# Optimization experiments

Hardware: AMD Instinct MI355X
Metric: run time of the kernel (lower is better)

The kernel has to match this reference:

```python
import jax, jax.numpy as jnp
import numpy as np

SCALE = 1.0 / np.sqrt(128.0)  # 1/sqrt(head_size)
NEG = -1000000000.0


def setup_inputs() -> dict:
    key = jax.random.key(0)
    k1, k2, k3, k4 = jax.random.split(key, 4)
    B, H, S, D = 2, 16, 2048, 128
    q = jax.random.normal(k1, (B, H, S, D), dtype=jnp.float32)
    k = jax.random.normal(k2, (B, H, S, D), dtype=jnp.float32)
    v = jax.random.normal(k3, (B, H, S, D), dtype=jnp.float32)
    mask = jax.random.randint(k4, (B, S), 0, 2, dtype=jnp.int32)
    return {"q": q, "k": k, "v": v, "mask": mask}


def reference(q, k, v, mask):
    # scores: [B, H, Sq, Sk]
    scores = jnp.einsum("bhqd,bhkd->bhqk", q, k) * SCALE
    m = mask[:, None, None, :]  # [B,1,1,Sk], broadcast over heads and queries
    scores = jnp.where(m == 0, NEG, scores)
    weights = jax.nn.softmax(scores, axis=-1)
    out = jnp.einsum("bhqk,bhkd->bhqd", weights, v)
    return out
```

## Files before the change

kernel.cpp:

```cpp
#include <hip/hip_runtime.h>
#include <hip/hip_bf16.h>

typedef __attribute__((ext_vector_type(8))) short short8;
typedef __attribute__((ext_vector_type(4))) short short4v;
typedef __attribute__((ext_vector_type(4))) float floatx4;

#define NBH 32
#define SS 2048
#define DD 128
#define BQ 128
#define BK 32
#define KTILES (SS / BK)
#define KPAIRS (KTILES / 2)
#define SCALE 0.08838834764831845f
#define LOG2E 1.4426950408889634f
#define MAXB 12.0f
#define MASKED_BIAS -100000.0f

#define WC_LGKM0 0xC07F

typedef union { float4 v; float f[4]; } f4u;

__device__ __forceinline__ short f2bf(float f) {
  union { float f; unsigned u; } x; x.f = f;
  return (short)((x.u + 0x7FFFu + ((x.u >> 16) & 1u)) >> 16);
}

__device__ __forceinline__ void pack8(short8* dst, float a, float b, float c, float d,
                                      float e, float f, float g, float h) {
  union { __hip_bfloat162 h2[4]; short8 v; } u;
  u.h2[0] = __float22bfloat162_rn(make_float2(a, b));
  u.h2[1] = __float22bfloat162_rn(make_float2(c, d));
  u.h2[2] = __float22bfloat162_rn(make_float2(e, f));
  u.h2[3] = __float22bfloat162_rn(make_float2(g, h));
  *dst = u.v;
}

__global__ __launch_bounds__(256, 2) void fa_kernel(
    const float* __restrict__ q, const float* __restrict__ k,
    const float* __restrict__ v, const int* __restrict__ mask,
    float* __restrict__ out) {
  __shared__ __align__(16) short Ks[4][BK * DD];
  __shared__ __align__(16) short Vt[4][DD * BK];
  __shared__ float Bias[SS];

  const int tid = threadIdx.x;
  const int wave = tid >> 6;
  const int lane = tid & 63;
  const int l16 = lane & 15;
  const int quad = lane >> 4;

  const int lid = blockIdx.y * 16 + blockIdx.x;
  const int vid = (lid & 7) * 64 + (lid >> 3);
  const int bh = vid >> 4;
  const int q0 = (vid & 15) * BQ;
  const int b = bh >> 4;
  const int poff = ((bh >> 1) & 1) << 4;

  const size_t base = (size_t)bh * SS * DD;
  const float* qg = q + base;
  const float* kg = k + base;
  const float* vg = v + base;
  const int* mg = mask + b * SS;
  const float c1 = SCALE * LOG2E, c2 = MAXB * LOG2E;

  const int krow = wave * 8 + (lane >> 3);
  const int kswr = krow & 7;
  const int kc0 = (lane & 7) * 2;
  const float* kldp = kg + (size_t)krow * DD + (lane & 7) * 16;
  const int kw0 = krow * DD + ((kc0 ^ kswr) * 8);
  const int kw1 = krow * DD + (((kc0 + 1) ^ kswr) * 8);
  const int kg4 = wave * 2 + (lane >> 5);
  const int dg = lane & 31;
  const int vgrp = kg4 & 3;
  const int vhalf = (kg4 >> 2) * 4;
  const float* vldp = vg + (size_t)(kg4 * 4) * DD + dg * 4;

  f4u kst[2][4], vst[2][4];

  {
    const int ktA = 2 * poff, ktB = ktA + 1;
#pragma unroll
    for (int i = 0; i < 4; ++i) {
      kst[0][i].v = *(const float4*)(kldp + (size_t)ktA * (BK * DD) + i * 4);
      kst[1][i].v = *(const float4*)(kldp + (size_t)ktB * (BK * DD) + i * 4);
    }
#pragma unroll
    for (int r = 0; r < 4; ++r) {
      vst[0][r].v = *(const float4*)(vldp + (size_t)ktA * (BK * DD) + r * DD);
      vst[1][r].v = *(const float4*)(vldp + (size_t)ktB * (BK * DD) + r * DD);
    }
  }

  short8 qf[2][4];
#pragma unroll
  for (int t = 0; t < 2; ++t) {
    const float* qp = qg + (size_t)(q0 + wave * 32 + t * 16 + l16) * DD;
#pragma unroll
    for (int dc = 0; dc < 4; ++dc) {
      float4 a = *(const float4*)(qp + dc * 32 + quad * 8);
      float4 bb = *(const float4*)(qp + dc * 32 + quad * 8 + 4);
      short8 tt;
      tt[0] = f2bf(a.x); tt[1] = f2bf(a.y); tt[2] = f2bf(a.z); tt[3] = f2bf(a.w);
      tt[4] = f2bf(bb.x); tt[5] = f2bf(bb.y); tt[6] = f2bf(bb.z); tt[7] = f2bf(bb.w);
      qf[t][dc] = tt;
    }
  }

  {
    int i0 = tid * 8;
    int4 m0 = *(const int4*)(mg + i0);
    int4 m1 = *(const int4*)(mg + i0 + 4);
    float4 f0, f1;
    f0.x = m0.x ? -c2 : MASKED_BIAS; f0.y = m0.y ? -c2 : MASKED_BIAS;
    f0.z = m0.z ? -c2 : MASKED_BIAS; f0.w = m0.w ? -c2 : MASKED_BIAS;
    f1.x = m1.x ? -c2 : MASKED_BIAS; f1.y = m1.y ? -c2 : MASKED_BIAS;
    f1.z = m1.z ? -c2 : MASKED_BIAS; f1.w = m1.w ? -c2 : MASKED_BIAS;
    *(float4*)&Bias[i0] = f0;
    *(float4*)&Bias[i0 + 4] = f1;
  }

#define WRITE_K(T, BUF)                                                        \
  {                                                                            \
    short8 lo_, hi_;                                                           \
    pack8(&lo_, kst[T][0].f[0], kst[T][0].f[1], kst[T][0].f[2], kst[T][0].f[3],\
          kst[T][1].f[0], kst[T][1].f[1], kst[T][1].f[2], kst[T][1].f[3]);     \
    pack8(&hi_, kst[T][2].f[0], kst[T][2].f[1], kst[T][2].f[2], kst[T][2].f[3],\
          kst[T][3].f[0], kst[T][3].f[1], kst[T][3].f[2], kst[T][3].f[3]);     \
    *(short8*)&Ks[BUF][kw0] = lo_;                                             \
    *(short8*)&Ks[BUF][kw1] = hi_;                                             \
  }

#define WRITE_V(T, BUF)                                                        \
  {                                                                            \
    _Pragma("unroll")                                                          \
    for (int j = 0; j < 4; ++j) {                                              \
      int d_ = dg * 4 + j;                                                     \
      int slot_ = ((vgrp ^ ((d_ >> 1) & 3)) * 8) + vhalf;                      \
      union { __hip_bfloat162 h2[2]; short4v s; } w_;                          \
      w_.h2[0] = __float22bfloat162_rn(make_float2(vst[T][0].f[j], vst[T][1].f[j])); \
      w_.h2[1] = __float22bfloat162_rn(make_float2(vst[T][2].f[j], vst[T][3].f[j])); \
      *(short4v*)&Vt[BUF][d_ * 32 + slot_] = w_.s;                             \
    }                                                                          \
  }

  WRITE_K(0, 0) WRITE_K(1, 1)
  WRITE_V(0, 0) WRITE_V(1, 1)
  __builtin_amdgcn_s_waitcnt(WC_LGKM0);
  __builtin_amdgcn_s_barrier();

  floatx4 Oacc[2][8];
#pragma unroll
  for (int t = 0; t < 2; ++t)
#pragma unroll
    for (int f = 0; f < 8; ++f) Oacc[t][f] = (floatx4){0.f, 0.f, 0.f, 0.f};
  float l_acc[2] = {0.f, 0.f};

  int koff[2];
#pragma unroll
  for (int nt = 0; nt < 2; ++nt) koff[nt] = (nt * 16 + l16) * DD;
  const int ksw = l16 & 7;
  const int voff = l16 * 32 + ((quad ^ ((l16 >> 1) & 3)) * 8);

#pragma unroll 1
  for (int j = 0; j < KPAIRS; ++j) {
    const int pp = (j + poff) & (KPAIRS - 1);
    const int ktA = 2 * pp, ktB = ktA + 1;
    const int tbA = 2 * (j & 1), tbB = tbA + 1;
    const int nxA = 2 * ((j + 1) & 1), nxB = nxA + 1;
    const short* ksA = &Ks[tbA][0];
    const short* ksB = &Ks[tbB][0];
    const short* vsA = &Vt[tbA][0];
    const short* vsB = &Vt[tbB][0];
    const int ppn = (j + 1 + poff) & (KPAIRS - 1);
    const int ktnA = 2 * ppn, ktnB = ktnA + 1;

    if (j + 1 < KPAIRS) {
#pragma unroll
      for (int i = 0; i < 4; ++i) {
        kst[0][i].v = *(const float4*)(kldp + (size_t)ktnA * (BK * DD) + i * 4);
        kst[1][i].v = *(const float4*)(kldp + (size_t)ktnB * (BK * DD) + i * 4);
      }
      __builtin_amdgcn_sched_barrier(0);
    }

    floatx4 sA[2][2], sB[2][2];
#pragma unroll
    for (int t = 0; t < 2; ++t)
#pragma unroll
      for (int nt = 0; nt < 2; ++nt) {
        sA[t][nt] = (floatx4){0.f, 0.f, 0.f, 0.f};
        sB[t][nt] = (floatx4){0.f, 0.f, 0.f, 0.f};
      }
    __builtin_amdgcn_s_setprio(1);
#pragma unroll
    for (int nt = 0; nt < 2; ++nt)
#pragma unroll
      for (int dc = 0; dc < 4; ++dc) {
        short8 kf = *(const short8*)(ksA + koff[nt] + (((dc * 4 + quad) ^ ksw) * 8));
        sA[0][nt] = __builtin_amdgcn_mfma_f32_16x16x32_bf16(kf, qf[0][dc], sA[0][nt], 0, 0, 0);
        sA[1][nt] = __builtin_amdgcn_mfma_f32_16x16x32_bf16(kf, qf[1][dc], sA[1][nt], 0, 0, 0);
      }
#pragma unroll
    for (int nt = 0; nt < 2; ++nt)
#pragma unroll
      for (int dc = 0; dc < 4; ++dc) {
        short8 kf = *(const short8*)(ksB + koff[nt] + (((dc * 4 + quad) ^ ksw) * 8));
        sB[0][nt] = __builtin_amdgcn_mfma_f32_16x16x32_bf16(kf, qf[0][dc], sB[0][nt], 0, 0, 0);
        sB[1][nt] = __builtin_amdgcn_mfma_f32_16x16x32_bf16(kf, qf[1][dc], sB[1][nt], 0, 0, 0);
      }
    __builtin_amdgcn_s_setprio(0);

    if (j + 1 < KPAIRS) {
      WRITE_K(0, nxA) WRITE_K(1, nxB)
#pragma unroll
      for (int r = 0; r < 4; ++r) {
        vst[0][r].v = *(const float4*)(vldp + (size_t)ktnA * (BK * DD) + r * DD);
        vst[1][r].v = *(const float4*)(vldp + (size_t)ktnB * (BK * DD) + r * DD);
      }
      __builtin_amdgcn_sched_barrier(0);
    }

    float4 bbA0 = *(const float4*)&Bias[ktA * 32 + quad * 4];
    float4 bbA1 = *(const float4*)&Bias[ktA * 32 + 16 + quad * 4];
    short8 pbA[2];
#pragma unroll
    for (int t = 0; t < 2; ++t) {
      float e0 = __builtin_amdgcn_exp2f(fmaf(sA[t][0][0], c1, bbA0.x));
      float e1 = __builtin_amdgcn_exp2f(fmaf(sA[t][0][1], c1, bbA0.y));
      float e2 = __builtin_amdgcn_exp2f(fmaf(sA[t][0][2], c1, bbA0.z));
      float e3 = __builtin_amdgcn_exp2f(fmaf(sA[t][0][3], c1, bbA0.w));
      float g0 = __builtin_amdgcn_exp2f(fmaf(sA[t][1][0], c1, bbA1.x));
      float g1 = __builtin_amdgcn_exp2f(fmaf(sA[t][1][1], c1, bbA1.y));
      float g2 = __builtin_amdgcn_exp2f(fmaf(sA[t][1][2], c1, bbA1.z));
      float g3 = __builtin_amdgcn_exp2f(fmaf(sA[t][1][3], c1, bbA1.w));
      l_acc[t] += ((e0 + e1) + (e2 + e3)) + ((g0 + g1) + (g2 + g3));
      pack8(&pbA[t], e0, e1, e2, e3, g0, g1, g2, g3);
    }

    __builtin_amdgcn_s_setprio(1);
#pragma unroll
    for (int f = 0; f < 8; ++f) {
      short8 vv = *(const short8*)(vsA + f * 512 + voff);
      Oacc[0][f] = __builtin_amdgcn_mfma_f32_16x16x32_bf16(vv, pbA[0], Oacc[0][f], 0, 0, 0);
      Oacc[1][f] = __builtin_amdgcn_mfma_f32_16x16x32_bf16(vv, pbA[1], Oacc[1][f], 0, 0, 0);
    }
    __builtin_amdgcn_s_setprio(0);

    float4 bbB0 = *(const float4*)&Bias[ktB * 32 + quad * 4];
    float4 bbB1 = *(const float4*)&Bias[ktB * 32 + 16 + quad * 4];
    short8 pbB[2];
#pragma unroll
    for (int t = 0; t < 2; ++t) {
      float e0 = __builtin_amdgcn_exp2f(fmaf(sB[t][0][0], c1, bbB0.x));
      float e1 = __builtin_amdgcn_exp2f(fmaf(sB[t][0][1], c1, bbB0.y));
      float e2 = __builtin_amdgcn_exp2f(fmaf(sB[t][0][2], c1, bbB0.z));
      float e3 = __builtin_amdgcn_exp2f(fmaf(sB[t][0][3], c1, bbB0.w));
      float g0 = __builtin_amdgcn_exp2f(fmaf(sB[t][1][0], c1, bbB1.x));
      float g1 = __builtin_amdgcn_exp2f(fmaf(sB[t][1][1], c1, bbB1.y));
      float g2 = __builtin_amdgcn_exp2f(fmaf(sB[t][1][2], c1, bbB1.z));
      float g3 = __builtin_amdgcn_exp2f(fmaf(sB[t][1][3], c1, bbB1.w));
      l_acc[t] += ((e0 + e1) + (e2 + e3)) + ((g0 + g1) + (g2 + g3));
      pack8(&pbB[t], e0, e1, e2, e3, g0, g1, g2, g3);
    }

    __builtin_amdgcn_s_setprio(1);
#pragma unroll
    for (int f = 0; f < 8; ++f) {
      short8 vv = *(const short8*)(vsB + f * 512 + voff);
      Oacc[0][f] = __builtin_amdgcn_mfma_f32_16x16x32_bf16(vv, pbB[0], Oacc[0][f], 0, 0, 0);
      Oacc[1][f] = __builtin_amdgcn_mfma_f32_16x16x32_bf16(vv, pbB[1], Oacc[1][f], 0, 0, 0);
    }
    __builtin_amdgcn_s_setprio(0);

    if (j + 1 < KPAIRS) {
      WRITE_V(0, nxA) WRITE_V(1, nxB)
      __builtin_amdgcn_s_waitcnt(WC_LGKM0);
      __builtin_amdgcn_s_barrier();
    }
  }
#undef WRITE_K
#undef WRITE_V

  float* og = out + base;
#pragma unroll
  for (int t = 0; t < 2; ++t) {
    float s = l_acc[t];
    s += __shfl_xor(s, 16);
    s += __shfl_xor(s, 32);
    float inv = 1.0f / s;
    float* orow = og + (size_t)(q0 + wave * 32 + t * 16 + l16) * DD + quad * 4;
#pragma unroll
    for (int f = 0; f < 8; ++f) {
      float4 w;
      w.x = Oacc[t][f][0] * inv;
      w.y = Oacc[t][f][1] * inv;
      w.z = Oacc[t][f][2] * inv;
      w.w = Oacc[t][f][3] * inv;
      *(float4*)(orow + f * 16) = w;
    }
  }
}

extern "C" void kernel_launch(void* const* d_in, const int* in_sizes, int n_in,
                              void* d_out, int out_size, void* d_ws, size_t ws_size,
                              hipStream_t stream) {
  const float* q = (const float*)d_in[0];
  const float* k = (const float*)d_in[1];
  const float* v = (const float*)d_in[2];
  const int* mask = (const int*)d_in[3];
  float* out = (float*)d_out;

  fa_kernel<<<dim3(SS / BQ, NBH), dim3(256), 0, stream>>>(q, k, v, mask, out);
}
```

Measured before the change: 220.8 us.

## Remap K/V staging so each lane writes one contiguous 16-byte LDS chunk

Reassigns which global elements each lane loads for K and V so that every lane writes exactly one 16-byte, linearly indexed LDS chunk per tile. The global reads are pre-swizzled to match the reading layout. K keeps vectorised float4 loads. V now uses scalar strided loads, a transposed gather, which replaces the earlier scattered 8-byte LDS stores. The goal is cheaper, conflict-free LDS writes, at the cost of more, less coalesced global load instructions for V.

```diff
diff --git a/kernel.cpp b/kernel.cpp
--- a/kernel.cpp
+++ b/kernel.cpp
@@ -64,32 +64,80 @@
   const int* mg = mask + b * SS;
   const float c1 = SCALE * LOG2E, c2 = MAXB * LOG2E;
 
-  const int krow = wave * 8 + (lane >> 3);
-  const int kswr = krow & 7;
-  const int kc0 = (lane & 7) * 2;
-  const float* kldp = kg + (size_t)krow * DD + (lane & 7) * 16;
-  const int kw0 = krow * DD + ((kc0 ^ kswr) * 8);
-  const int kw1 = krow * DD + (((kc0 + 1) ^ kswr) * 8);
-  const int kg4 = wave * 2 + (lane >> 5);
-  const int dg = lane & 31;
-  const int vgrp = kg4 & 3;
-  const int vhalf = (kg4 >> 2) * 4;
-  const float* vldp = vg + (size_t)(kg4 * 4) * DD + dg * 4;
-
-  f4u kst[2][4], vst[2][4];
+  const float* ksrc[2];
+  const float* vsrc[2][2];
+  int si[2];
+#pragma unroll
+  for (int p = 0; p < 2; ++p) {
+    const int kr = wave * 8 + p * 4 + (lane >> 4);
+    const int kgc = (lane & 15) ^ (kr & 7);
+    ksrc[p] = kg + (size_t)kr * DD + kgc * 8;
+    const int vd = wave * 32 + p * 16 + (lane >> 2);
+    const int vgc = (lane & 3) ^ ((vd >> 1) & 3);
+    vsrc[p][0] = vg + (size_t)(vgc * 4) * DD + vd;
+    vsrc[p][1] = vg + (size_t)(16 + vgc * 4) * DD + vd;
+    si[p] = wave * 1024 + p * 512 + lane * 8;
+  }
+
+  f4u kld[2][2][2];
+  float vld[2][2][8];
+
+#define LOAD_K(KTA_, KTB_)                                                     \
+  {                                                                            \
+    _Pragma("unroll")                                                          \
+    for (int p = 0; p < 2; ++p) {                                              \
+      const float* a0 = ksrc[p] + (size_t)(KTA_) * (BK * DD);                  \
+      const float* a1 = ksrc[p] + (size_t)(KTB_) * (BK * DD);                  \
+      kld[0][p][0].v = *(const float4*)a0;                                     \
+      kld[0][p][1].v = *(const float4*)(a0 + 4);                               \
+      kld[1][p][0].v = *(const float4*)a1;                                     \
+      kld[1][p][1].v = *(const float4*)(a1 + 4);                               \
+    }                                                                          \
+  }
+
+#define LOAD_V(KTA_, KTB_)                                                     \
+  {                                                                            \
+    _Pragma("unroll")                                                          \
+    for (int p = 0; p < 2; ++p)                                                \
+      _Pragma("unroll")                                                        \
+      for (int h = 0; h < 2; ++h) {                                            \
+        const float* b0 = vsrc[p][h] + (size_t)(KTA_) * (BK * DD);             \
+        const float* b1 = vsrc[p][h] + (size_t)(KTB_) * (BK * DD);             \
+        _Pragma("unroll")                                                      \
+        for (int rr = 0; rr < 4; ++rr) {                                       \
+          vld[0][p][h * 4 + rr] = b0[rr * DD];                                 \
+          vld[1][p][h * 4 + rr] = b1[rr * DD];                                 \
+        }                                                                      \
+      }                                                                        \
+  }
+
+#define WRITE_K(T, BUF)                                                        \
+  {                                                                            \
+    _Pragma("unroll")                                                          \
+    for (int p = 0; p < 2; ++p) {                                              \
+      short8 s_;                                                               \
+      pack8(&s_, kld[T][p][0].f[0], kld[T][p][0].f[1], kld[T][p][0].f[2],      \
+            kld[T][p][0].f[3], kld[T][p][1].f[0], kld[T][p][1].f[1],           \
+            kld[T][p][1].f[2], kld[T][p][1].f[3]);                             \
+      *(short8*)&Ks[BUF][si[p]] = s_;                                          \
+    }                                                                          \
+  }
+
+#define WRITE_V(T, BUF)                                                        \
+  {                                                                            \
+    _Pragma("unroll")                                                          \
+    for (int p = 0; p < 2; ++p) {                                              \
+      short8 s_;                                                               \
+      pack8(&s_, vld[T][p][0], vld[T][p][1], vld[T][p][2], vld[T][p][3],       \
+            vld[T][p][4], vld[T][p][5], vld[T][p][6], vld[T][p][7]);           \
+      *(short8*)&Vt[BUF][si[p]] = s_;                                          \
+    }                                                                          \
+  }
 
   {
-    const int ktA = 2 * poff, ktB = ktA + 1;
-#pragma unroll
-    for (int i = 0; i < 4; ++i) {
-      kst[0][i].v = *(const float4*)(kldp + (size_t)ktA * (BK * DD) + i * 4);
-      kst[1][i].v = *(const float4*)(kldp + (size_t)ktB * (BK * DD) + i * 4);
-    }
-#pragma unroll
-    for (int r = 0; r < 4; ++r) {
-      vst[0][r].v = *(const float4*)(vldp + (size_t)ktA * (BK * DD) + r * DD);
-      vst[1][r].v = *(const float4*)(vldp + (size_t)ktB * (BK * DD) + r * DD);
-    }
+    const int pp0 = poff & (KPAIRS - 1);
+    LOAD_K(2 * pp0, 2 * pp0 + 1)
+    LOAD_V(2 * pp0, 2 * pp0 + 1)
   }
 
   short8 qf[2][4];
@@ -118,30 +166,6 @@
     f1.z = m1.z ? -c2 : MASKED_BIAS; f1.w = m1.w ? -c2 : MASKED_BIAS;
     *(float4*)&Bias[i0] = f0;
     *(float4*)&Bias[i0 + 4] = f1;
-  }
-
-#define WRITE_K(T, BUF)                                                        \
-  {                                                                            \
-    short8 lo_, hi_;                                                           \
-    pack8(&lo_, kst[T][0].f[0], kst[T][0].f[1], kst[T][0].f[2], kst[T][0].f[3],\
-          kst[T][1].f[0], kst[T][1].f[1], kst[T][1].f[2], kst[T][1].f[3]);     \
-    pack8(&hi_, kst[T][2].f[0], kst[T][2].f[1], kst[T][2].f[2], kst[T][2].f[3],\
-          kst[T][3].f[0], kst[T][3].f[1], kst[T][3].f[2], kst[T][3].f[3]);     \
-    *(short8*)&Ks[BUF][kw0] = lo_;                                             \
-    *(short8*)&Ks[BUF][kw1] = hi_;                                             \
-  }
-
-#define WRITE_V(T, BUF)                                                        \
-  {                                                                            \
-    _Pragma("unroll")                                                          \
-    for (int j = 0; j < 4; ++j) {                                              \
-      int d_ = dg * 4 + j;                                                     \
-      int slot_ = ((vgrp ^ ((d_ >> 1) & 3)) * 8) + vhalf;                      \
-      union { __hip_bfloat162 h2[2]; short4v s; } w_;                          \
-      w_.h2[0] = __float22bfloat162_rn(make_float2(vst[T][0].f[j], vst[T][1].f[j])); \
-      w_.h2[1] = __float22bfloat162_rn(make_float2(vst[T][2].f[j], vst[T][3].f[j])); \
-      *(short4v*)&Vt[BUF][d_ * 32 + slot_] = w_.s;                             \
-    }                                                                          \
   }
 
   WRITE_K(0, 0) WRITE_K(1, 1)
@@ -176,11 +200,7 @@
     const int ktnA = 2 * ppn, ktnB = ktnA + 1;
 
     if (j + 1 < KPAIRS) {
-#pragma unroll
-      for (int i = 0; i < 4; ++i) {
-        kst[0][i].v = *(const float4*)(kldp + (size_t)ktnA * (BK * DD) + i * 4);
-        kst[1][i].v = *(const float4*)(kldp + (size_t)ktnB * (BK * DD) + i * 4);
-      }
+      LOAD_K(ktnA, ktnB)
       __builtin_amdgcn_sched_barrier(0);
     }
 
@@ -213,11 +233,7 @@
 
     if (j + 1 < KPAIRS) {
       WRITE_K(0, nxA) WRITE_K(1, nxB)
-#pragma unroll
-      for (int r = 0; r < 4; ++r) {
-        vst[0][r].v = *(const float4*)(vldp + (size_t)ktnA * (BK * DD) + r * DD);
-        vst[1][r].v = *(const float4*)(vldp + (size_t)ktnB * (BK * DD) + r * DD);
-      }
+      LOAD_V(ktnA, ktnB)
       __builtin_amdgcn_sched_barrier(0);
     }
 
@@ -279,6 +295,8 @@
       __builtin_amdgcn_s_barrier();
     }
   }
+#undef LOAD_K
+#undef LOAD_V
 #undef WRITE_K
 #undef WRITE_V
 
```

New measurement: 248.6 us. 1.13x slower.
